# Kernel optimization log

Measured on AMD Instinct MI355X. Metric: run time of the kernel, lower is better.

The kernel has to match this reference:

```python
import math
import jax, jax.numpy as jnp
import numpy as np

D_MODEL = 1024
N_HEAD = 16
HEAD_DIM = D_MODEL // N_HEAD
T = 1.0
EPS = 1e-5  # torch LayerNorm default


def _layernorm(t, gamma, beta):
    # normalize over last dim (head_dim)
    m = t.mean(axis=-1, keepdims=True)
    var = ((t - m) ** 2).mean(axis=-1, keepdims=True)
    return (t - m) * jax.lax.rsqrt(var + EPS) * gamma + beta


def setup_inputs() -> dict:
    key = jax.random.key(0)
    k1, k2, k3 = jax.random.split(key, 3)
    B, S = 4, 2048
    scale = 1.0 / math.sqrt(D_MODEL)
    return {
        "x": jax.random.normal(k1, (B, S, D_MODEL), dtype=jnp.float32),
        "w_qkv": jax.random.normal(k2, (D_MODEL, 3 * D_MODEL), dtype=jnp.float32) * scale,
        "w_proj": jax.random.normal(k3, (D_MODEL, D_MODEL), dtype=jnp.float32) * scale,
        "q_gamma": jnp.ones((HEAD_DIM,), dtype=jnp.float32),
        "q_beta": jnp.zeros((HEAD_DIM,), dtype=jnp.float32),
        "k_gamma": jnp.ones((HEAD_DIM,), dtype=jnp.float32),
        "k_beta": jnp.zeros((HEAD_DIM,), dtype=jnp.float32),
    }


def reference(x, w_qkv, w_proj, q_gamma, q_beta, k_gamma, k_beta):
    B, S, C = x.shape
    H, Dh = N_HEAD, HEAD_DIM
    # QKV projection -> [3, B, H, S, Dh]
    qkv = (x @ w_qkv).reshape(B, S, 3, H, Dh)
    qkv = jnp.transpose(qkv, (2, 0, 3, 1, 4))
    q, k, v = qkv[0], qkv[1], qkv[2]
    # per-head QK LayerNorm
    q = _layernorm(q, q_gamma, q_beta)
    k = _layernorm(k, k_gamma, k_beta)
    # temperature-scaled attention; jax.nn.softmax performs the stable
    # max-subtraction the original does explicitly
    logits = jnp.einsum("bhsd,bhtd->bhst", q, k) / (math.sqrt(Dh) * T)
    att = jax.nn.softmax(logits, axis=-1)
    out = jnp.einsum("bhst,bhtd->bhsd", att, v)
    out = jnp.transpose(out, (0, 2, 1, 3)).reshape(B, S, C)
    return out @ w_proj
```

## Files before the change

### kernel.cpp

```cpp
#include <hip/hip_runtime.h>
#include <stdint.h>

#define D_MODEL 1024
#define NHEAD 16
#define HDIM 64
#define BATCH 4
#define SEQ 2048
#define BS (BATCH*SEQ)
#define NQKV (3*D_MODEL)
#define BHEADS (BATCH*NHEAD)

typedef __bf16 bf16x8 __attribute__((ext_vector_type(8)));
typedef __bf16 bf16x2 __attribute__((ext_vector_type(2)));
typedef float f32x4 __attribute__((ext_vector_type(4)));
typedef float f32x2 __attribute__((ext_vector_type(2)));
typedef float f32x16 __attribute__((ext_vector_type(16)));

__device__ __forceinline__ unsigned short f2bf(float f) {
    union { __bf16 b; unsigned short s; } u; u.b = (__bf16)f; return u.s;
}
__device__ __forceinline__ float bf2f(unsigned short b) {
    union { unsigned u; float f; } v; v.u = ((unsigned)b) << 16;
    return v.f;
}
__device__ __forceinline__ unsigned pack_bf16(float a, float b) {
    f32x2 t; t[0] = a; t[1] = b;
    bf16x2 r = __builtin_convertvector(t, bf16x2);
    union { bf16x2 v; unsigned u; } u; u.v = r; return u.u;
}

typedef __attribute__((address_space(3))) void lds_void_t;
typedef const __attribute__((address_space(1))) void glb_void_t;
__device__ __forceinline__ void gl2lds16(const void* g, void* l) {
    __builtin_amdgcn_global_load_lds((glb_void_t*)g, (lds_void_t*)l, 16, 0, 0);
}

__global__ __launch_bounds__(256) void k_cvt_x(const float4* __restrict__ x,
                                               uint2* __restrict__ o) {
    int i = blockIdx.x * 256 + threadIdx.x;
    float4 v = x[i];
    uint2 r;
    r.x = (unsigned)f2bf(v.x) | ((unsigned)f2bf(v.y) << 16);
    r.y = (unsigned)f2bf(v.z) | ((unsigned)f2bf(v.w) << 16);
    o[i] = r;
}

__global__ __launch_bounds__(256) void k_transpose(const float* __restrict__ in,
                                                   unsigned short* __restrict__ out,
                                                   int ndim) {
    __shared__ float tile[64][65];
    const int n0 = blockIdx.x * 64, k0 = blockIdx.y * 64, tid = threadIdx.x;
#pragma unroll
    for (int i = 0; i < 16; i++) {
        int f = i * 256 + tid; int r = f >> 6, c = f & 63;
        tile[r][c] = in[(size_t)(k0 + r) * ndim + n0 + c];
    }
    __syncthreads();
#pragma unroll
    for (int i = 0; i < 16; i++) {
        int f = i * 256 + tid; int n = f >> 6, kq = f & 63;
        out[(size_t)(n0 + n) * 1024 + k0 + kq] = f2bf(tile[kq][n]);
    }
}

template<int MODE>
__global__ __launch_bounds__(256) void k_gemm(const unsigned short* __restrict__ A,
                                              const unsigned short* __restrict__ Bt,
                                              float* __restrict__ Cout,
                                              unsigned short* __restrict__ qo,
                                              unsigned short* __restrict__ ko,
                                              unsigned short* __restrict__ vo) {
    __shared__ __align__(16) unsigned short As[128 * 64];
    __shared__ __align__(16) unsigned short Bs[128 * 64];
    const int tid = threadIdx.x, lane = tid & 63, wid = tid >> 6;
    const int l16 = lane & 15, lq = lane >> 4;
    const int wr = wid >> 1, wc = wid & 1;
    const int M0 = blockIdx.x * 128, N0 = blockIdx.y * 128;

    f32x4 acc[4][4] = {};

    for (int k0 = 0; k0 < 1024; k0 += 64) {
#pragma unroll
        for (int i = 0; i < 4; i++) {
            int ch = i * 256 + tid;
            int r = ch >> 3, c = (ch & 7) * 8;
            int ldsbase = (i * 256 + wid * 64) * 8;
            gl2lds16(A  + (size_t)(M0 + r) * 1024 + k0 + c, &As[ldsbase]);
            gl2lds16(Bt + (size_t)(N0 + r) * 1024 + k0 + c, &Bs[ldsbase]);
        }
        __syncthreads();
#pragma unroll
        for (int kk = 0; kk < 2; kk++) {
            bf16x8 af[4], bfr[4];
#pragma unroll
            for (int m = 0; m < 4; m++)
                af[m] = *(const bf16x8*)&As[(wr * 64 + m * 16 + l16) * 64 + kk * 32 + lq * 8];
#pragma unroll
            for (int n = 0; n < 4; n++)
                bfr[n] = *(const bf16x8*)&Bs[(wc * 64 + n * 16 + l16) * 64 + kk * 32 + lq * 8];
#pragma unroll
            for (int m = 0; m < 4; m++)
#pragma unroll
                for (int n = 0; n < 4; n++)
                    acc[m][n] = __builtin_amdgcn_mfma_f32_16x16x32_bf16(af[m], bfr[n], acc[m][n], 0, 0, 0);
        }
        __syncthreads();
    }

#pragma unroll
    for (int m = 0; m < 4; m++) {
#pragma unroll
        for (int n = 0; n < 4; n++) {
#pragma unroll
            for (int r = 0; r < 4; r++) {
                int row = M0 + wr * 64 + m * 16 + lq * 4 + r;
                int col = N0 + wc * 64 + n * 16 + l16;
                float val = acc[m][n][r];
                if (MODE == 1) {
                    Cout[(size_t)row * 1024 + col] = val;
                } else {
                    int which = col >> 10, h = (col >> 6) & 15, d = col & 63;
                    int b = row >> 11, s = row & 2047, bh = (b << 4) + h;
                    unsigned short bv = f2bf(val);
                    size_t off = ((size_t)bh * SEQ + s) * 64 + d;
                    if (which == 0)      qo[off] = bv;
                    else if (which == 1) ko[off] = bv;
                    else                 vo[off] = bv;
                }
            }
        }
    }
}

__global__ __launch_bounds__(256) void k_vtr(const unsigned short* __restrict__ v,
                                             unsigned short* __restrict__ vt) {
    __shared__ __align__(16) unsigned short tile[64][70];
    const int tid = threadIdx.x;
    const int s0 = blockIdx.x * 64, bh = blockIdx.y;
    const unsigned short* src = v + ((size_t)bh * SEQ + s0) * 64;
#pragma unroll
    for (int i = 0; i < 2; i++) {
        int ch = i * 256 + tid; int r = ch >> 3, c = (ch & 7) * 8;
        *(bf16x8*)&tile[r][c] = *(const bf16x8*)(src + r * 64 + c);
    }
    __syncthreads();
    unsigned short* dst = vt + (size_t)bh * 64 * SEQ + s0;
#pragma unroll
    for (int i = 0; i < 2; i++) {
        int ch = i * 256 + tid; int d = ch >> 3, sc = (ch & 7) * 8;
        ushort4 a, b;
        a.x = tile[sc + 0][d]; a.y = tile[sc + 1][d];
        a.z = tile[sc + 2][d]; a.w = tile[sc + 3][d];
        b.x = tile[sc + 4][d]; b.y = tile[sc + 5][d];
        b.z = tile[sc + 6][d]; b.w = tile[sc + 7][d];
        *(ushort4*)(dst + (size_t)d * SEQ + sc) = a;
        *(ushort4*)(dst + (size_t)d * SEQ + sc + 4) = b;
    }
}

__global__ __launch_bounds__(256) void k_ln(unsigned short* __restrict__ q,
                                            unsigned short* __restrict__ k,
                                            const float* __restrict__ qg, const float* __restrict__ qb,
                                            const float* __restrict__ kg, const float* __restrict__ kb) {
    const int wid = threadIdx.x >> 6, lane = threadIdx.x & 63;
    size_t row = (size_t)blockIdx.x * 4 + wid;
    unsigned short* p = blockIdx.y ? k : q;
    const float* g  = blockIdx.y ? kg : qg;
    const float* bb = blockIdx.y ? kb : qb;
    const float c = blockIdx.y ? 1.0f : 0.18033688011112042f;
    float v = bf2f(p[row * 64 + lane]);
    float s = v;
#pragma unroll
    for (int m = 32; m; m >>= 1) s += __shfl_xor(s, m);
    float mean = s * (1.0f / 64.0f);
    float d = v - mean, sq = d * d;
#pragma unroll
    for (int m = 32; m; m >>= 1) sq += __shfl_xor(sq, m);
    float rs = rsqrtf(sq * (1.0f / 64.0f) + 1e-5f);
    p[row * 64 + lane] = f2bf((d * rs * g[lane] + bb[lane]) * c);
}

__global__ __launch_bounds__(256, 4) void k_flash(const unsigned short* __restrict__ q,
                                                  const unsigned short* __restrict__ k,
                                                  const unsigned short* __restrict__ vt,
                                                  unsigned short* __restrict__ aout) {
    __shared__ __align__(16) unsigned short Ks[2][64 * 64];
    __shared__ __align__(16) unsigned short Vs[2][64 * 64];
    const int tid = threadIdx.x, lane = tid & 63, wid = tid >> 6;
    const int l32 = lane & 31, hi = lane >> 5;
    const int bh = blockIdx.x;
    const int q0 = blockIdx.y * 128 + wid * 32;

    const unsigned short* qrow = q + ((size_t)bh * SEQ + q0 + l32) * 64 + hi * 8;
    bf16x8 bq[4];
#pragma unroll
    for (int t = 0; t < 4; t++)
        bq[t] = *(const bf16x8*)(qrow + t * 16);

    const unsigned short* kp[2];
    const unsigned short* vp[2];
#pragma unroll
    for (int i = 0; i < 2; i++) {
        int s = i * 256 + tid;
        int row = s >> 3, gsrc = (s & 7) ^ (row & 7);
        kp[i] = k  + (size_t)bh * SEQ * 64 + (size_t)row * 64  + gsrc * 8;
        vp[i] = vt + (size_t)bh * 64 * SEQ + (size_t)row * SEQ + gsrc * 8;
    }
#pragma unroll
    for (int i = 0; i < 2; i++) {
        int ldsoff = (i * 256 + wid * 64) * 8;
        gl2lds16(kp[i], &Ks[0][ldsoff]);
        gl2lds16(vp[i], &Vs[0][ldsoff]);
        kp[i] += 64 * 64; vp[i] += 64;
    }
    __syncthreads();

    f32x16 o0 = {}, o1 = {};
    float m_run = -1e30f, l_run = 0.f;
    const int xs = (l32 & 7);

    for (int t = 0; t < SEQ / 64; t++) {
        const int cur = t & 1;
        if (t + 1 < SEQ / 64) {
#pragma unroll
            for (int i = 0; i < 2; i++) {
                int ldsoff = (i * 256 + wid * 64) * 8;
                gl2lds16(kp[i], &Ks[cur ^ 1][ldsoff]);
                gl2lds16(vp[i], &Vs[cur ^ 1][ldsoff]);
                kp[i] += 64 * 64; vp[i] += 64;
            }
        }

        f32x16 sa0 = {}, sa1 = {};
        __builtin_amdgcn_s_setprio(1);
#pragma unroll
        for (int ks = 0; ks < 4; ks++) {
            int gx = (((ks * 2 + hi) ^ xs) * 8);
            bf16x8 ak0 = *(const bf16x8*)&Ks[cur][l32 * 64 + gx];
            bf16x8 ak1 = *(const bf16x8*)&Ks[cur][(32 + l32) * 64 + gx];
            sa0 = __builtin_amdgcn_mfma_f32_32x32x16_bf16(ak0, bq[ks], sa0, 0, 0, 0);
            sa1 = __builtin_amdgcn_mfma_f32_32x32x16_bf16(ak1, bq[ks], sa1, 0, 0, 0);
        }
        __builtin_amdgcn_s_setprio(0);

        float mx = fmaxf(sa0[0], sa1[0]);
#pragma unroll
        for (int r = 1; r < 16; r++) mx = fmaxf(mx, fmaxf(sa0[r], sa1[r]));
        mx = fmaxf(mx, __shfl_xor(mx, 32));

        if (!__all(mx <= m_run + 8.0f)) {
            float mn = fmaxf(m_run, mx);
            float sc = __builtin_amdgcn_exp2f(m_run - mn);
            o0 *= sc; o1 *= sc;
            l_run *= sc;
            m_run = mn;
        }

        float rs = 0.f;
#pragma unroll
        for (int r = 0; r < 16; r++) { sa0[r] = __builtin_amdgcn_exp2f(sa0[r] - m_run); rs += sa0[r]; }
#pragma unroll
        for (int r = 0; r < 16; r++) { sa1[r] = __builtin_amdgcn_exp2f(sa1[r] - m_run); rs += sa1[r]; }
        rs += __shfl_xor(rs, 32);
        l_run += rs;

        union BP { unsigned w[4]; bf16x8 v; };
        BP bpf[4];
#pragma unroll
        for (int ks = 0; ks < 4; ks++) {
            const f32x16& ps = (ks >> 1) ? sa1 : sa0;
            const int base = (ks & 1) * 8;
            unsigned a0 = pack_bf16(ps[base + 0], ps[base + 1]);
            unsigned a1 = pack_bf16(ps[base + 2], ps[base + 3]);
            unsigned b0 = pack_bf16(ps[base + 4], ps[base + 5]);
            unsigned b1 = pack_bf16(ps[base + 6], ps[base + 7]);
            asm volatile("v_permlane32_swap_b32 %0, %1" : "+v"(a0), "+v"(b0));
            asm volatile("v_permlane32_swap_b32 %0, %1" : "+v"(a1), "+v"(b1));
            bpf[ks].w[0] = a0; bpf[ks].w[1] = a1; bpf[ks].w[2] = b0; bpf[ks].w[3] = b1;
        }

        __builtin_amdgcn_s_setprio(1);
#pragma unroll
        for (int ks = 0; ks < 4; ks++) {
            int gx = (((ks * 2 + hi) ^ xs) * 8);
            bf16x8 av0 = *(const bf16x8*)&Vs[cur][l32 * 64 + gx];
            bf16x8 av1 = *(const bf16x8*)&Vs[cur][(32 + l32) * 64 + gx];
            o0 = __builtin_amdgcn_mfma_f32_32x32x16_bf16(av0, bpf[ks].v, o0, 0, 0, 0);
            o1 = __builtin_amdgcn_mfma_f32_32x32x16_bf16(av1, bpf[ks].v, o1, 0, 0, 0);
        }
        __builtin_amdgcn_s_setprio(0);
        __syncthreads();
    }

    float inv = 1.0f / l_run;
    const int b = bh >> 4, h = bh & 15;
    unsigned short* orow = aout + ((size_t)b * SEQ + q0 + l32) * 1024 + h * 64;
#pragma unroll
    for (int dblk = 0; dblk < 2; dblk++) {
        const f32x16& oo = dblk ? o1 : o0;
#pragma unroll
        for (int q2 = 0; q2 < 4; q2++) {
            ushort4 u4;
            u4.x = f2bf(oo[q2 * 4 + 0] * inv);
            u4.y = f2bf(oo[q2 * 4 + 1] * inv);
            u4.z = f2bf(oo[q2 * 4 + 2] * inv);
            u4.w = f2bf(oo[q2 * 4 + 3] * inv);
            *(ushort4*)(orow + dblk * 32 + q2 * 8 + hi * 4) = u4;
        }
    }
}

extern "C" void kernel_launch(void* const* d_in, const int* in_sizes, int n_in,
                              void* d_out, int out_size, void* d_ws, size_t ws_size,
                              hipStream_t stream) {
    const float* x     = (const float*)d_in[0];
    const float* wqkv  = (const float*)d_in[1];
    const float* wproj = (const float*)d_in[2];
    const float* qg    = (const float*)d_in[3];
    const float* qb    = (const float*)d_in[4];
    const float* kg    = (const float*)d_in[5];
    const float* kb    = (const float*)d_in[6];
    float* out = (float*)d_out;

    char* ws = (char*)d_ws;
    unsigned short* xbf    = (unsigned short*)(ws);
    unsigned short* wqkvT  = (unsigned short*)(ws + (16llu << 20));
    unsigned short* wprojT = (unsigned short*)(ws + (22llu << 20));
    unsigned short* qraw   = (unsigned short*)(ws + (24llu << 20));
    unsigned short* kraw   = (unsigned short*)(ws + (40llu << 20));
    unsigned short* vraw   = (unsigned short*)(ws + (56llu << 20));
    unsigned short* aattn  = (unsigned short*)(ws + (72llu << 20));
    unsigned short* vtr    = xbf;

    hipLaunchKernelGGL(k_cvt_x, dim3(8192), dim3(256), 0, stream, (const float4*)x, (uint2*)xbf);
    hipLaunchKernelGGL(k_transpose, dim3(48, 16), dim3(256), 0, stream, wqkv, wqkvT, 3072);
    hipLaunchKernelGGL(k_transpose, dim3(16, 16), dim3(256), 0, stream, wproj, wprojT, 1024);
    hipLaunchKernelGGL((k_gemm<0>), dim3(64, 24), dim3(256), 0, stream, xbf, wqkvT, (float*)nullptr, qraw, kraw, vraw);
    hipLaunchKernelGGL(k_ln, dim3(32768, 2), dim3(256), 0, stream, qraw, kraw, qg, qb, kg, kb);
    hipLaunchKernelGGL(k_vtr, dim3(32, 64), dim3(256), 0, stream, vraw, vtr);
    hipLaunchKernelGGL(k_flash, dim3(64, 16), dim3(256), 0, stream, qraw, kraw, vtr, aattn);
    hipLaunchKernelGGL((k_gemm<1>), dim3(64, 8), dim3(256), 0, stream, aattn, wprojT, out,
                       (unsigned short*)nullptr, (unsigned short*)nullptr, (unsigned short*)nullptr);
}
```

Before: 258.0 us.

## Fuse QK LayerNorm into QKV GEMM epilogue and enlarge GEMM tiles

Removes the separate LayerNorm kernel and applies the per-head LayerNorm inside the QKV GEMM epilogue. Each wave's 64 output columns are exactly one head, so row statistics are reduced with lane shuffles. The GEMM block grows to 512 threads with a 256x128 tile, and a swizzled block index is added for cache locality. This drops a full read and write pass over Q and K plus one launch. In exchange the GEMM uses more LDS per block, runs at lower occupancy, and computes variance as E[x^2]-mean^2 in fp32 before rounding to bf16.

```diff
diff --git a/kernel.cpp b/kernel.cpp
--- a/kernel.cpp
+++ b/kernel.cpp
@@ -64,28 +64,44 @@
 }
 
 template<int MODE>
-__global__ __launch_bounds__(256) void k_gemm(const unsigned short* __restrict__ A,
-                                              const unsigned short* __restrict__ Bt,
-                                              float* __restrict__ Cout,
-                                              unsigned short* __restrict__ qo,
-                                              unsigned short* __restrict__ ko,
-                                              unsigned short* __restrict__ vo) {
-    __shared__ __align__(16) unsigned short As[128 * 64];
+__global__ __launch_bounds__(512, 6) void k_gemm(const unsigned short* __restrict__ A,
+                                                 const unsigned short* __restrict__ Bt,
+                                                 float* __restrict__ Cout,
+                                                 unsigned short* __restrict__ qo,
+                                                 unsigned short* __restrict__ ko,
+                                                 unsigned short* __restrict__ vo,
+                                                 const float* __restrict__ qg,
+                                                 const float* __restrict__ qb,
+                                                 const float* __restrict__ kg,
+                                                 const float* __restrict__ kb,
+                                                 int nbx) {
+    __shared__ __align__(16) unsigned short As[256 * 64];
     __shared__ __align__(16) unsigned short Bs[128 * 64];
     const int tid = threadIdx.x, lane = tid & 63, wid = tid >> 6;
     const int l16 = lane & 15, lq = lane >> 4;
     const int wr = wid >> 1, wc = wid & 1;
-    const int M0 = blockIdx.x * 128, N0 = blockIdx.y * 128;
+
+    const int nwg = nbx * gridDim.y;
+    int bid = blockIdx.x + nbx * blockIdx.y;
+    int swz = (bid & 7) * (nwg >> 3) + (bid >> 3);
+    const int bx = swz % nbx, by = swz / nbx;
+    const int M0 = bx * 256, N0 = by * 128;
 
     f32x4 acc[4][4] = {};
 
     for (int k0 = 0; k0 < 1024; k0 += 64) {
 #pragma unroll
         for (int i = 0; i < 4; i++) {
-            int ch = i * 256 + tid;
-            int r = ch >> 3, c = (ch & 7) * 8;
-            int ldsbase = (i * 256 + wid * 64) * 8;
-            gl2lds16(A  + (size_t)(M0 + r) * 1024 + k0 + c, &As[ldsbase]);
+            int g = i * 512 + tid;
+            int r = g >> 3, c = (g & 7) * 8;
+            int ldsbase = (i * 512 + wid * 64) * 8;
+            gl2lds16(A + (size_t)(M0 + r) * 1024 + k0 + c, &As[ldsbase]);
+        }
+#pragma unroll
+        for (int i = 0; i < 2; i++) {
+            int g = i * 512 + tid;
+            int r = g >> 3, c = (g & 7) * 8;
+            int ldsbase = (i * 512 + wid * 64) * 8;
             gl2lds16(Bt + (size_t)(N0 + r) * 1024 + k0 + c, &Bs[ldsbase]);
         }
         __syncthreads();
@@ -107,26 +123,77 @@
         __syncthreads();
     }
 
+    if (MODE == 1) {
+#pragma unroll
+        for (int m = 0; m < 4; m++)
+#pragma unroll
+            for (int n = 0; n < 4; n++)
+#pragma unroll
+                for (int r = 0; r < 4; r++) {
+                    int row = M0 + wr * 64 + m * 16 + lq * 4 + r;
+                    int col = N0 + wc * 64 + n * 16 + l16;
+                    Cout[(size_t)row * 1024 + col] = acc[m][n][r];
+                }
+        return;
+    }
+
+    const int colbase = N0 + wc * 64;
+    const int which = colbase >> 10;
+    const int h = (colbase >> 6) & 15;
+    const int b = M0 >> 11;
+    const int bh = (b << 4) + h;
+    const int srow0 = (M0 & 2047) + wr * 64;
+
+    if (which == 2) {
+#pragma unroll
+        for (int m = 0; m < 4; m++)
+#pragma unroll
+            for (int n = 0; n < 4; n++)
+#pragma unroll
+                for (int r = 0; r < 4; r++) {
+                    int s = srow0 + m * 16 + lq * 4 + r;
+                    int d = n * 16 + l16;
+                    vo[((size_t)bh * SEQ + s) * 64 + d] = f2bf(acc[m][n][r]);
+                }
+        return;
+    }
+
+    unsigned short* outp = which ? ko : qo;
+    const float* gp = which ? kg : qg;
+    const float* bp = which ? kb : qb;
+    const float cs = which ? 1.0f : 0.18033688011112042f;
+    float gv[4], bv[4];
+#pragma unroll
+    for (int n = 0; n < 4; n++) { gv[n] = gp[n * 16 + l16]; bv[n] = bp[n * 16 + l16]; }
+
 #pragma unroll
     for (int m = 0; m < 4; m++) {
+        f32x4 s1 = acc[m][0] + acc[m][1] + acc[m][2] + acc[m][3];
+        f32x4 s2 = acc[m][0] * acc[m][0] + acc[m][1] * acc[m][1]
+                 + acc[m][2] * acc[m][2] + acc[m][3] * acc[m][3];
+#pragma unroll
+        for (int mask = 1; mask < 16; mask <<= 1) {
+#pragma unroll
+            for (int r = 0; r < 4; r++) {
+                s1[r] += __shfl_xor(s1[r], mask);
+                s2[r] += __shfl_xor(s2[r], mask);
+            }
+        }
+        f32x4 mean = s1 * 0.015625f;
+        f32x4 rstd;
+#pragma unroll
+        for (int r = 0; r < 4; r++) {
+            float var = s2[r] * 0.015625f - mean[r] * mean[r];
+            rstd[r] = rsqrtf(var + 1e-5f);
+        }
 #pragma unroll
         for (int n = 0; n < 4; n++) {
+            int d = n * 16 + l16;
 #pragma unroll
             for (int r = 0; r < 4; r++) {
-                int row = M0 + wr * 64 + m * 16 + lq * 4 + r;
-                int col = N0 + wc * 64 + n * 16 + l16;
-                float val = acc[m][n][r];
-                if (MODE == 1) {
-                    Cout[(size_t)row * 1024 + col] = val;
-                } else {
-                    int which = col >> 10, h = (col >> 6) & 15, d = col & 63;
-                    int b = row >> 11, s = row & 2047, bh = (b << 4) + h;
-                    unsigned short bv = f2bf(val);
-                    size_t off = ((size_t)bh * SEQ + s) * 64 + d;
-                    if (which == 0)      qo[off] = bv;
-                    else if (which == 1) ko[off] = bv;
-                    else                 vo[off] = bv;
-                }
+                int s = srow0 + m * 16 + lq * 4 + r;
+                float val = ((acc[m][n][r] - mean[r]) * rstd[r] * gv[n] + bv[n]) * cs;
+                outp[((size_t)bh * SEQ + s) * 64 + d] = f2bf(val);
             }
         }
     }
@@ -156,28 +223,6 @@
         *(ushort4*)(dst + (size_t)d * SEQ + sc) = a;
         *(ushort4*)(dst + (size_t)d * SEQ + sc + 4) = b;
     }
-}
-
-__global__ __launch_bounds__(256) void k_ln(unsigned short* __restrict__ q,
-                                            unsigned short* __restrict__ k,
-                                            const float* __restrict__ qg, const float* __restrict__ qb,
-                                            const float* __restrict__ kg, const float* __restrict__ kb) {
-    const int wid = threadIdx.x >> 6, lane = threadIdx.x & 63;
-    size_t row = (size_t)blockIdx.x * 4 + wid;
-    unsigned short* p = blockIdx.y ? k : q;
-    const float* g  = blockIdx.y ? kg : qg;
-    const float* bb = blockIdx.y ? kb : qb;
-    const float c = blockIdx.y ? 1.0f : 0.18033688011112042f;
-    float v = bf2f(p[row * 64 + lane]);
-    float s = v;
-#pragma unroll
-    for (int m = 32; m; m >>= 1) s += __shfl_xor(s, m);
-    float mean = s * (1.0f / 64.0f);
-    float d = v - mean, sq = d * d;
-#pragma unroll
-    for (int m = 32; m; m >>= 1) sq += __shfl_xor(sq, m);
-    float rs = rsqrtf(sq * (1.0f / 64.0f) + 1e-5f);
-    p[row * 64 + lane] = f2bf((d * rs * g[lane] + bb[lane]) * c);
 }
 
 __global__ __launch_bounds__(256, 4) void k_flash(const unsigned short* __restrict__ q,
@@ -335,10 +380,11 @@
     hipLaunchKernelGGL(k_cvt_x, dim3(8192), dim3(256), 0, stream, (const float4*)x, (uint2*)xbf);
     hipLaunchKernelGGL(k_transpose, dim3(48, 16), dim3(256), 0, stream, wqkv, wqkvT, 3072);
     hipLaunchKernelGGL(k_transpose, dim3(16, 16), dim3(256), 0, stream, wproj, wprojT, 1024);
-    hipLaunchKernelGGL((k_gemm<0>), dim3(64, 24), dim3(256), 0, stream, xbf, wqkvT, (float*)nullptr, qraw, kraw, vraw);
-    hipLaunchKernelGGL(k_ln, dim3(32768, 2), dim3(256), 0, stream, qraw, kraw, qg, qb, kg, kb);
+    hipLaunchKernelGGL((k_gemm<0>), dim3(32, 24), dim3(512), 0, stream, xbf, wqkvT, (float*)nullptr,
+                       qraw, kraw, vraw, qg, qb, kg, kb, 32);
     hipLaunchKernelGGL(k_vtr, dim3(32, 64), dim3(256), 0, stream, vraw, vtr);
     hipLaunchKernelGGL(k_flash, dim3(64, 16), dim3(256), 0, stream, qraw, kraw, vtr, aattn);
-    hipLaunchKernelGGL((k_gemm<1>), dim3(64, 8), dim3(256), 0, stream, aattn, wprojT, out,
-                       (unsigned short*)nullptr, (unsigned short*)nullptr, (unsigned short*)nullptr);
-}
+    hipLaunchKernelGGL((k_gemm<1>), dim3(32, 8), dim3(512), 0, stream, aattn, wprojT, out,
+                       (unsigned short*)nullptr, (unsigned short*)nullptr, (unsigned short*)nullptr,
+                       (const float*)nullptr, (const float*)nullptr, (const float*)nullptr, (const float*)nullptr, 32);
+}
```

After: 782.2 us. 3.03x slower.
